# Performance work log

Measured on AMD Instinct MI355X. Metric: run time of the kernel, lower is better.

## Reference

```python
import jax, jax.numpy as jnp
import numpy as np

VOCAB, EMB, ATT = 100000, 128, 128
N_CODES, N_ANC = 100000, 8

def setup_inputs() -> dict:
    key = jax.random.key(0)
    k1, k2, k3, k4, k5 = jax.random.split(key, 5)
    return {
        "W_emb": jax.random.normal(k1, (VOCAB, EMB), dtype=jnp.float32),
        "W_attention": jax.random.normal(k2, (2 * EMB, ATT), dtype=jnp.float32) * 0.05,
        "b_attention": jnp.zeros((ATT,), dtype=jnp.float32),
        "v_attention": jax.random.normal(k3, (ATT,), dtype=jnp.float32) * 0.05,
        "leaves": jax.random.randint(k4, (N_CODES, N_ANC), 0, VOCAB, dtype=jnp.int64),
        "ancestors": jax.random.randint(k5, (N_CODES, N_ANC), 0, VOCAB, dtype=jnp.int64),
    }

def reference(W_emb, W_attention, b_attention, v_attention, leaves, ancestors):
    # gather: [N, A, E] each
    leave_emb = W_emb[leaves]
    anc_emb = W_emb[ancestors]
    attention_input = jnp.concatenate((leave_emb, anc_emb), axis=2)  # [N, A, 2E]
    mlp = jnp.tanh(jnp.einsum('nae,ed->nad', attention_input, W_attention) + b_attention)
    pre_attention = jnp.einsum('nad,d->na', mlp, v_attention)  # [N, A]
    attn = jax.nn.softmax(pre_attention, axis=1)
    # attention-weighted sum over ancestors: [N, E]
    return jnp.einsum('nae,na->ne', anc_emb, attn)
```

## Files before the change

kernel.cpp:

```cpp
#include <hip/hip_runtime.h>
#include <hip/hip_bf16.h>
#include <hip/hip_fp8.h>

#define VOCAB  100000
#define EMB    128
#define NCODES 100000
#define NANC   8

#define ATT_GRID 625
#define ATT_TPB  5
#define PRE_GRID 1250
#define PRE_TPB  5

typedef __attribute__((ext_vector_type(8))) short    short8;
typedef __attribute__((ext_vector_type(4))) float    float4v;
typedef __attribute__((ext_vector_type(2))) float    floatx2;
typedef __attribute__((ext_vector_type(4))) unsigned uint4v;
typedef __attribute__((ext_vector_type(2))) __bf16   bf16x2;

__device__ __forceinline__ ushort f2bf(float x) {
    unsigned u = __float_as_uint(x);
    u += 0x7fffu + ((u >> 16) & 1u);
    return (ushort)(u >> 16);
}
__device__ __forceinline__ float bf2f(ushort h) {
    return __uint_as_float((unsigned)h << 16);
}
__device__ __forceinline__ unsigned pk2bf(float lo, float hi) {
    bf16x2 v;
    v[0] = (__bf16)lo;
    v[1] = (__bf16)hi;
    return __builtin_bit_cast(unsigned, v);
}
__device__ __forceinline__ unsigned char f2fp8(float x) {
    __hip_fp8_e4m3 t(x);
    return t.__x;
}
__device__ __forceinline__ unsigned pack_fp8x4(float a, float b, float c, float d) {
#if __has_builtin(__builtin_amdgcn_cvt_pk_fp8_f32)
    int w = __builtin_amdgcn_cvt_pk_fp8_f32(a, b, 0, false);
    w = __builtin_amdgcn_cvt_pk_fp8_f32(c, d, w, true);
    return (unsigned)w;
#else
    return (unsigned)f2fp8(a) | ((unsigned)f2fp8(b) << 8)
         | ((unsigned)f2fp8(c) << 16) | ((unsigned)f2fp8(d) << 24);
#endif
}
template <bool HI>
__device__ __forceinline__ floatx2 fp8pair(unsigned v) {
#if __has_builtin(__builtin_amdgcn_cvt_pk_f32_fp8)
    return __builtin_amdgcn_cvt_pk_f32_fp8((int)v, HI);
#else
    __hip_fp8_e4m3 a, b;
    const unsigned s = HI ? 16u : 0u;
    a.__x = (v >> s) & 0xffu;
    b.__x = (v >> (s + 8u)) & 0xffu;
    floatx2 r; r[0] = (float)a; r[1] = (float)b; return r;
#endif
}

__device__ __forceinline__ void tanh2pk(floatx2 za, floatx2 zb,
                                        floatx2& ta, floatx2& tb) {
    floatx2 xa, xb;
    xa[0] = fminf(fmaxf(za[0], -3.5f), 3.5f);
    xa[1] = fminf(fmaxf(za[1], -3.5f), 3.5f);
    xb[0] = fminf(fmaxf(zb[0], -3.5f), 3.5f);
    xb[1] = fminf(fmaxf(zb[1], -3.5f), 3.5f);
    const floatx2 ya = xa * xa, yb = xb * xb;
    floatx2 Na = ya + 105.0f;  Na = ya * Na + 945.0f;
    floatx2 Nb = yb + 105.0f;  Nb = yb * Nb + 945.0f;
    floatx2 Da = ya * 15.0f + 420.0f;  Da = ya * Da + 945.0f;
    floatx2 Db = yb * 15.0f + 420.0f;  Db = yb * Db + 945.0f;
    const floatx2 Dp = Da * Db;
    const float r = __builtin_amdgcn_rcpf(Dp[0] * Dp[1]);
    floatx2 qv;  qv[0] = r * Dp[1];  qv[1] = r * Dp[0];
    const floatx2 ia = qv * Db;
    const floatx2 ib = qv * Da;
    ta = (xa * Na) * ia;
    tb = (xb * Nb) * ib;
}

__global__ void transpose_watt(const float* __restrict__ W_att,
                               ushort* __restrict__ WT)
{
    const int id = blockIdx.x * 256 + threadIdx.x;
    const int c = id >> 7, e = id & 127;
    const int h = c >> 7, d = c & 127;
    WT[c * 128 + e] = f2bf(W_att[(h * 128 + e) * 128 + d]);
}

__global__ __launch_bounds__(256) void precompute(
    const float*  __restrict__ W_emb,
    const ushort* __restrict__ WT,
    const float*  __restrict__ b_att,
    unsigned char* __restrict__ P1,
    unsigned char* __restrict__ M)
{
    const int t = threadIdx.x, wave = t >> 6, lane = t & 63;
    const int n15 = lane & 15, quad = lane >> 4;
    const int cw = wave * 64;

    short8 wfrag[4][4];
    #pragma unroll
    for (int ntl = 0; ntl < 4; ++ntl) {
        const int c = cw + ((n15 >> 2) << 4) + ntl * 4 + (n15 & 3);
        #pragma unroll
        for (int kt = 0; kt < 4; ++kt)
            wfrag[kt][ntl] = *(const short8*)(WT + c * 128 + kt * 32 + quad * 8);
    }

    float4 bb[4];
    #pragma unroll
    for (int ntl = 0; ntl < 4; ++ntl) {
        if (wave < 2) bb[ntl] = *(const float4*)(b_att + cw + quad * 16 + ntl * 4);
        else          bb[ntl] = make_float4(0.f, 0.f, 0.f, 0.f);
    }

    unsigned char* Pt;
    size_t rstride;
    int cbase;
    if (wave < 2) { Pt = P1; rstride = 128; cbase = cw + quad * 16; }
    else          { Pt = M;  rstride = 384; cbase = (cw - 128) + quad * 16; }

    const int b = blockIdx.x;

#define LOAD_TILE(dst, rtv)                                                   \
    {                                                                         \
        const float4v* src =                                                  \
            (const float4v*)(W_emb + (size_t)((rtv) * 16 + n15) * 128);       \
        _Pragma("unroll")                                                     \
        for (int kt = 0; kt < 4; ++kt) {                                      \
            (dst)[2 * kt]     = __builtin_nontemporal_load(src + kt * 8 + quad * 2);     \
            (dst)[2 * kt + 1] = __builtin_nontemporal_load(src + kt * 8 + quad * 2 + 1); \
        }                                                                     \
    }

    float4v buf[3][8];
    LOAD_TILE(buf[0], b)
    LOAD_TILE(buf[1], b + PRE_GRID)

    #pragma unroll
    for (int it = 0; it < PRE_TPB; ++it) {
        if (it + 2 < PRE_TPB)
            LOAD_TILE(buf[(it + 2) % 3], b + (it + 2) * PRE_GRID)

        const float4v* cur = buf[it % 3];
        const int R = (b + it * PRE_GRID) * 16;

        float4v acc[4];
        #pragma unroll
        for (int i = 0; i < 4; ++i) acc[i] = (float4v)0.0f;

        #pragma unroll
        for (int kt = 0; kt < 4; ++kt) {
            const float4v a0 = cur[2 * kt], a1 = cur[2 * kt + 1];
            uint4v ad;
            ad[0] = pk2bf(a0[0], a0[1]);
            ad[1] = pk2bf(a0[2], a0[3]);
            ad[2] = pk2bf(a1[0], a1[1]);
            ad[3] = pk2bf(a1[2], a1[3]);
            const short8 af = __builtin_bit_cast(short8, ad);
            if ((wave < 2) && ((kt >> 1) == wave))
                *(short8*)(M + (size_t)(R + n15) * 384 + 128 + kt * 64 + quad * 16) = af;
            #pragma unroll
            for (int ntl = 0; ntl < 4; ++ntl)
                acc[ntl] = __builtin_amdgcn_mfma_f32_16x16x32_bf16(
                               wfrag[kt][ntl], af, acc[ntl], 0, 0, 0);
        }

        uint4v pks;
        #pragma unroll
        for (int ntl = 0; ntl < 4; ++ntl)
            pks[ntl] = pack_fp8x4(acc[ntl][0] + bb[ntl].x,
                                  acc[ntl][1] + bb[ntl].y,
                                  acc[ntl][2] + bb[ntl].z,
                                  acc[ntl][3] + bb[ntl].w);
        *(uint4v*)(Pt + (size_t)(R + n15) * rstride + cbase) = pks;
    }
#undef LOAD_TILE
}

__global__ __launch_bounds__(256) void attention_main(
    const unsigned char* __restrict__ P1,
    const unsigned char* __restrict__ M,
    const float* __restrict__ v_att,
    const int*   __restrict__ leaves, const int* __restrict__ anc,
    float*       __restrict__ out, int tile0)
{
    const int t = threadIdx.x;
    const int wave = t >> 6, lane = t & 63;
    const int sub = lane >> 4, l16 = lane & 15;
    const int jj = l16 & 7;

    floatx2 vv[4];
    #pragma unroll
    for (int p = 0; p < 4; ++p)
        vv[p] = *(const floatx2*)(v_att + l16 * 8 + 2 * p);

    const int base = tile0 + blockIdx.x;

    auto idx_ptr = [&](int tile) -> const int* {
        const int n = tile * 16 + wave * 4 + sub;
        return (l16 & 8) ? (anc + n * 8 + jj) : (leaves + n * 8 + jj);
    };

    int    lf[2][NANC], an[2][NANC];
    uint2  R1[2][NANC], R2[2][NANC];
    short8 EM[NANC];
    int    raw[2];

    raw[0] = __builtin_nontemporal_load(idx_ptr(base));
    #pragma unroll
    for (int a = 0; a < NANC; ++a) {
        lf[0][a] = __shfl(raw[0], (sub << 4) + a);
        an[0][a] = __shfl(raw[0], (sub << 4) + 8 + a);
    }
    #pragma unroll
    for (int a = 0; a < NANC; ++a)
        R1[0][a] = *(const uint2*)(P1 + (size_t)lf[0][a] * 128 + l16 * 8);
    #pragma unroll
    for (int a = 0; a < NANC; ++a)
        R2[0][a] = *(const uint2*)(M + (size_t)an[0][a] * 384 + l16 * 8);
    #pragma unroll
    for (int a = 0; a < NANC; ++a)
        EM[a] = *(const short8*)(M + (size_t)an[0][a] * 384 + 128 + l16 * 16);
    raw[1] = __builtin_nontemporal_load(idx_ptr(base + ATT_GRID));

    #pragma unroll
    for (int it = 0; it < ATT_TPB; ++it) {
        const int cur = it & 1, nx = cur ^ 1;
        const int tile = base + it * ATT_GRID;

        if (it + 1 < ATT_TPB) {
            #pragma unroll
            for (int a = 0; a < NANC; ++a) {
                lf[nx][a] = __shfl(raw[nx], (sub << 4) + a);
                an[nx][a] = __shfl(raw[nx], (sub << 4) + 8 + a);
            }
            #pragma unroll
            for (int a = 0; a < NANC; ++a)
                R1[nx][a] = *(const uint2*)(P1 + (size_t)lf[nx][a] * 128 + l16 * 8);
            #pragma unroll
            for (int a = 0; a < NANC; ++a)
                R2[nx][a] = *(const uint2*)(M + (size_t)an[nx][a] * 384 + l16 * 8);
        }
        if (it + 2 < ATT_TPB)
            raw[cur] = __builtin_nontemporal_load(idx_ptr(tile + 2 * ATT_GRID));

        const int n = tile * 16 + wave * 4 + sub;

        float q[NANC];
        #pragma unroll
        for (int a = 0; a < NANC; ++a) {
            const floatx2 z0 = fp8pair<false>(R1[cur][a].x) + fp8pair<false>(R2[cur][a].x);
            const floatx2 z1 = fp8pair<true >(R1[cur][a].x) + fp8pair<true >(R2[cur][a].x);
            const floatx2 z2 = fp8pair<false>(R1[cur][a].y) + fp8pair<false>(R2[cur][a].y);
            const floatx2 z3 = fp8pair<true >(R1[cur][a].y) + fp8pair<true >(R2[cur][a].y);
            floatx2 t0, t1, t2, t3;
            tanh2pk(z0, z1, t0, t1);
            tanh2pk(z2, z3, t2, t3);
            floatx2 qa = t0 * vv[0];
            qa = t1 * vv[1] + qa;
            qa = t2 * vv[2] + qa;
            qa = t3 * vv[3] + qa;
            q[a] = qa[0] + qa[1];
        }

        float r4[4];
        #pragma unroll
        for (int i = 0; i < 4; ++i) {
            const float keep = (l16 & 8) ? q[i + 4] : q[i];
            const float send = (l16 & 8) ? q[i]     : q[i + 4];
            r4[i] = keep + __shfl_xor(send, 8);
        }
        float s2[2];
        #pragma unroll
        for (int i = 0; i < 2; ++i) {
            const float keep = (l16 & 4) ? r4[i + 2] : r4[i];
            const float send = (l16 & 4) ? r4[i]     : r4[i + 2];
            s2[i] = keep + __shfl_xor(send, 4);
        }
        {
            const float keep = (l16 & 2) ? s2[1] : s2[0];
            const float send = (l16 & 2) ? s2[0] : s2[1];
            s2[0] = keep + __shfl_xor(send, 2);
        }
        float tq = s2[0] + __shfl_xor(s2[0], 1);

        float m = tq;
        m = fmaxf(m, __shfl_xor(m, 8));
        m = fmaxf(m, __shfl_xor(m, 4));
        m = fmaxf(m, __shfl_xor(m, 2));
        const float e = __expf(tq - m);
        float s = e;
        s += __shfl_xor(s, 8); s += __shfl_xor(s, 4); s += __shfl_xor(s, 2);
        const float wl = e * __fdividef(1.0f, s);

        float wa[NANC];
        {
            const float p  = __shfl_xor(wl, 2);
            const float w0 = (l16 & 2) ? p  : wl;
            const float w1 = (l16 & 2) ? wl : p;
            const float p0 = __shfl_xor(w0, 4), p1 = __shfl_xor(w1, 4);
            const float v00 = (l16 & 4) ? p0 : w0, v01 = (l16 & 4) ? p1 : w1;
            const float v10 = (l16 & 4) ? w0 : p0, v11 = (l16 & 4) ? w1 : p1;
            float g;
            g = __shfl_xor(v00, 8); wa[0] = (l16 & 8) ? g : v00; wa[4] = (l16 & 8) ? v00 : g;
            g = __shfl_xor(v01, 8); wa[1] = (l16 & 8) ? g : v01; wa[5] = (l16 & 8) ? v01 : g;
            g = __shfl_xor(v10, 8); wa[2] = (l16 & 8) ? g : v10; wa[6] = (l16 & 8) ? v10 : g;
            g = __shfl_xor(v11, 8); wa[3] = (l16 & 8) ? g : v11; wa[7] = (l16 & 8) ? v11 : g;
        }

        floatx2 o[4] = {(floatx2)0.f, (floatx2)0.f, (floatx2)0.f, (floatx2)0.f};
        #pragma unroll
        for (int a = 0; a < NANC; ++a) {
            floatx2 wv; wv[0] = wa[a]; wv[1] = wa[a];
            #pragma unroll
            for (int p = 0; p < 4; ++p) {
                floatx2 ev;
                ev[0] = bf2f((ushort)EM[a][2 * p]);
                ev[1] = bf2f((ushort)EM[a][2 * p + 1]);
                o[p] = ev * wv + o[p];
            }
        }
        float4v o1, o2;
        o1[0] = o[0][0]; o1[1] = o[0][1]; o1[2] = o[1][0]; o1[3] = o[1][1];
        o2[0] = o[2][0]; o2[1] = o[2][1]; o2[2] = o[3][0]; o2[3] = o[3][1];
        __builtin_nontemporal_store(o1, (float4v*)(out + (size_t)n * 128 + l16 * 8));
        __builtin_nontemporal_store(o2, (float4v*)(out + (size_t)n * 128 + l16 * 8 + 4));

        if (it + 1 < ATT_TPB) {
            #pragma unroll
            for (int a = 0; a < NANC; ++a)
                EM[a] = *(const short8*)(M + (size_t)an[nx][a] * 384 + 128 + l16 * 16);
        }
    }
}

extern "C" void kernel_launch(void* const* d_in, const int* in_sizes, int n_in,
                              void* d_out, int out_size, void* d_ws, size_t ws_size,
                              hipStream_t stream) {
    const float* W_emb  = (const float*)d_in[0];
    const float* W_att  = (const float*)d_in[1];
    const float* b_att  = (const float*)d_in[2];
    const float* v_att  = (const float*)d_in[3];
    const int*   leaves = (const int*)d_in[4];
    const int*   anc    = (const int*)d_in[5];
    float*       out    = (float*)d_out;

    unsigned char* P1 = (unsigned char*)d_ws;
    unsigned char* M  = P1 + (size_t)VOCAB * 128;
    ushort* WT = (ushort*)(M + (size_t)VOCAB * 384);

    transpose_watt<<<128, 256, 0, stream>>>(W_att, WT);
    precompute<<<PRE_GRID, 256, 0, stream>>>(W_emb, WT, b_att, P1, M);
    attention_main<<<ATT_GRID, 256, 0, stream>>>(P1, M, v_att,
                                                 leaves, anc, out, 0);
    attention_main<<<ATT_GRID, 256, 0, stream>>>(P1, M, v_att,
                                                 leaves, anc, out, 3125);
}
```

Baseline: 215.6 us.

## Stage embedding tiles through LDS once per block instead of per-wave register loads

New measurement: 196.0 us. -9.1%, faster.

```diff
diff --git a/kernel.cpp b/kernel.cpp
--- a/kernel.cpp
+++ b/kernel.cpp
@@ -96,6 +96,8 @@
     unsigned char* __restrict__ P1,
     unsigned char* __restrict__ M)
 {
+    __shared__ __align__(16) float lds[2048];
+
     const int t = threadIdx.x, wave = t >> 6, lane = t & 63;
     const int n15 = lane & 15, quad = lane >> 4;
     const int cw = wave * 64;
@@ -124,36 +126,40 @@
 
     const int b = blockIdx.x;
 
-#define LOAD_TILE(dst, rtv)                                                   \
-    {                                                                         \
-        const float4v* src =                                                  \
-            (const float4v*)(W_emb + (size_t)((rtv) * 16 + n15) * 128);       \
-        _Pragma("unroll")                                                     \
-        for (int kt = 0; kt < 4; ++kt) {                                      \
-            (dst)[2 * kt]     = __builtin_nontemporal_load(src + kt * 8 + quad * 2);     \
-            (dst)[2 * kt + 1] = __builtin_nontemporal_load(src + kt * 8 + quad * 2 + 1); \
-        }                                                                     \
-    }
-
-    float4v buf[3][8];
-    LOAD_TILE(buf[0], b)
-    LOAD_TILE(buf[1], b + PRE_GRID)
+    const int r0 = t >> 5, cf = (t & 31) * 4;
 
     #pragma unroll
     for (int it = 0; it < PRE_TPB; ++it) {
-        if (it + 2 < PRE_TPB)
-            LOAD_TILE(buf[(it + 2) % 3], b + (it + 2) * PRE_GRID)
-
-        const float4v* cur = buf[it % 3];
-        const int R = (b + it * PRE_GRID) * 16;
-
+        const int rt = b + it * PRE_GRID;
+        const float* tb0 = W_emb + (size_t)rt * 2048;
+
+#if __has_builtin(__builtin_amdgcn_global_load_lds)
+        __builtin_amdgcn_global_load_lds(
+            (const __attribute__((address_space(1))) void*)(tb0 + r0 * 128 + cf),
+            (__attribute__((address_space(3))) void*)&lds[wave * 256],
+            16, 0, 0);
+        __builtin_amdgcn_global_load_lds(
+            (const __attribute__((address_space(1))) void*)(tb0 + (r0 + 8) * 128 + cf),
+            (__attribute__((address_space(3))) void*)&lds[1024 + wave * 256],
+            16, 0, 0);
+        asm volatile("s_waitcnt vmcnt(0)" ::: "memory");
+#else
+        const float4v v0 = *(const float4v*)(tb0 + r0 * 128 + cf);
+        const float4v v1 = *(const float4v*)(tb0 + (r0 + 8) * 128 + cf);
+        *(float4v*)&lds[t * 4]        = v0;
+        *(float4v*)&lds[1024 + t * 4] = v1;
+#endif
+        __syncthreads();
+
+        const int R = rt * 16;
         float4v acc[4];
         #pragma unroll
         for (int i = 0; i < 4; ++i) acc[i] = (float4v)0.0f;
 
         #pragma unroll
         for (int kt = 0; kt < 4; ++kt) {
-            const float4v a0 = cur[2 * kt], a1 = cur[2 * kt + 1];
+            const float4v a0 = *(const float4v*)&lds[n15 * 128 + kt * 32 + quad * 8];
+            const float4v a1 = *(const float4v*)&lds[n15 * 128 + kt * 32 + quad * 8 + 4];
             uint4v ad;
             ad[0] = pk2bf(a0[0], a0[1]);
             ad[1] = pk2bf(a0[2], a0[3]);
@@ -176,8 +182,10 @@
                                   acc[ntl][2] + bb[ntl].z,
                                   acc[ntl][3] + bb[ntl].w);
         *(uint4v*)(Pt + (size_t)(R + n15) * rstride + cbase) = pks;
-    }
-#undef LOAD_TILE
+
+        if (it + 1 < PRE_TPB)
+            __syncthreads();
+    }
 }
 
 __global__ __launch_bounds__(256) void attention_main(
```
